# Kernel optimization log

Measured on AMD Instinct MI355X. Metric: run time of the kernel, lower is better.

## Reference

```python
import jax, jax.numpy as jnp
import numpy as np
from jax.scipy.special import ndtri
from jax.scipy.stats import norm

B, C, S = 8192, 1024, 16  # batch, num_classes, sample_size


def setup_inputs() -> dict:
    key = jax.random.key(0)
    k1, k2 = jax.random.split(key)
    logits = jax.random.normal(k1, (B, C), dtype=jnp.float32)
    labels = jax.random.randint(k2, (B,), 0, C, dtype=jnp.int32)
    temperature = jnp.ones((1,), dtype=jnp.float32)
    return {"logits": logits, "labels": labels, "temperature": temperature}


def _exact_loss(logits, labels, temperature, sample_size=S):
    # Global batch-norm of logits (torch .std() is unbiased -> ddof=1).
    logits = (logits - logits.mean()) / jnp.std(logits, ddof=1)
    num_classes = logits.shape[-1]
    # logits_deltas: target logit minus every logit, target column excluded via mask.
    tgt = jnp.take_along_axis(logits, labels[:, None], axis=-1)  # (B, 1)
    delta = (tgt - logits) / temperature[0]                      # (B, C)
    alt_mask = 1.0 - jax.nn.one_hot(labels, num_classes, dtype=logits.dtype)  # 0 at target
    # PositiveNormalProb: P(delta_j + eps_y - eps_j > 0 for all j != y),
    # eps iid N(0,1). Conditioning on eps_y = t gives independent events:
    #   prob = E_{t~N(0,1)}[ prod_j Phi(delta_j + t) ]
    # integrated with sample_size midpoint quantile nodes t_k = Phi^{-1}((k+0.5)/S).
    grid = (jnp.arange(sample_size, dtype=logits.dtype) + 0.5) / sample_size
    t = ndtri(grid)                                              # (S,)
    logcdf = norm.logcdf(delta[:, None, :] + t[None, :, None])   # (B, S, C)
    logp = jnp.sum(logcdf * alt_mask[:, None, :], axis=-1)       # (B, S)
    probs = jnp.mean(jnp.exp(logp), axis=-1)                     # (B,)
    # reduction = 'mean': expected error rate
    return 1.0 - probs.mean()


def reference(logits, labels, temperature):
    return _exact_loss(logits, labels, temperature)
```

## Files before the change

### kernel.cpp

```cpp
#include <hip/hip_runtime.h>
#include <math.h>

#define NB 8192
#define NC 1024
#define NS 16

#define NT   2464
#define NTR  2461
#define C0   48
#define BMAXF 1984.0f
#define UBIAS 978.5f

constexpr int OFFK[16] = {0, 69, 109, 139, 164, 187, 208, 228,
                          248, 268, 289, 312, 337, 367, 407, 476};

#define PSUM  16
#define PSQ   1040
#define RCNT  2064
#define RLIST 3088
#define PART  11280
#define TAB   11408
#define NBLK_MAIN 128

__global__ __launch_bounds__(256) void k_pre(const float* __restrict__ logits,
                                             const int* __restrict__ labels,
                                             float* __restrict__ ws) {
    const int bid = blockIdx.x;
    if (bid >= 1024) {
        int i = (bid - 1024) * 256 + threadIdx.x;
        if (i < NT) {
            int ii = i < NTR ? i : (NTR - 1);
            double x = -9.5 + (double)ii * (1.0 / 128.0);
            ws[TAB + i] = (float)log(0.5 * erfc(-x * 0.70710678118654752440));
        }
        return;
    }
    const int w = threadIdx.x >> 6, l = threadIdx.x & 63;
    const float4* lf4 = (const float4*)logits;
    __shared__ int flags[8];
    __shared__ float bs[4], bss[4];
    float s = 0.0f, ss = 0.0f;
    for (int rr = 0; rr < 2; ++rr) {
        const int row = bid * 8 + w * 2 + rr;
        const float tgt = logits[row * NC + labels[row]];
        int cnt = 0;
        #pragma unroll
        for (int i = 0; i < 4; ++i) {
            float4 v = lf4[row * (NC / 4) + l + 64 * i];
            s  += v.x + v.y + v.z + v.w;
            ss += v.x * v.x + v.y * v.y + v.z * v.z + v.w * v.w;
            cnt += (v.x >= tgt) + (v.y >= tgt) + (v.z >= tgt) + (v.w >= tgt);
        }
        #pragma unroll
        for (int m = 32; m; m >>= 1) cnt += __shfl_xor(cnt, m, 64);
        if (l == 0) flags[w * 2 + rr] = ((cnt - 1) < C0);
    }
    #pragma unroll
    for (int m = 32; m; m >>= 1) {
        s  += __shfl_xor(s,  m, 64);
        ss += __shfl_xor(ss, m, 64);
    }
    if (l == 0) { bs[w] = s; bss[w] = ss; }
    __syncthreads();
    if (threadIdx.x == 0) {
        ws[PSUM + bid] = bs[0] + bs[1] + bs[2] + bs[3];
        ws[PSQ + bid]  = bss[0] + bss[1] + bss[2] + bss[3];
        int* wsi = (int*)ws;
        int n = 0;
        #pragma unroll
        for (int i = 0; i < 8; ++i)
            if (flags[i]) wsi[RLIST + bid * 8 + (n++)] = bid * 8 + i;
        wsi[RCNT + bid] = n;
    }
}

__global__ __launch_bounds__(256) void k_main(const float* __restrict__ logits,
                                              const int* __restrict__ labels,
                                              const float* __restrict__ temp,
                                              float* __restrict__ ws) {
    const int bid = blockIdx.x, tid = threadIdx.x;
    const int* wsi = (const int*)ws;
    const int w = tid >> 6, l = tid & 63;

    __shared__ float lt[NT];
    __shared__ int   P[1024];
    __shared__ int   wtot[4];
    __shared__ float rs[4], rss[4];
    __shared__ float shInv;
    __shared__ float wprob[4];

    float4* lt4 = (float4*)lt;
    const float4* gt4 = (const float4*)(ws + TAB);
    for (int i = tid; i < NT / 4; i += 256) lt4[i] = gt4[i];

    int c4[4];
    const int b4 = tid * 4;
    #pragma unroll
    for (int j = 0; j < 4; ++j) c4[j] = wsi[RCNT + b4 + j];
    int s4 = c4[0] + c4[1] + c4[2] + c4[3];
    int v = s4;
    #pragma unroll
    for (int off = 1; off < 64; off <<= 1) {
        int u = __shfl_up(v, off, 64);
        if (l >= off) v += u;
    }
    if (l == 63) wtot[w] = v;

    float s  = ws[PSUM + tid] + ws[PSUM + 256 + tid] + ws[PSUM + 512 + tid] + ws[PSUM + 768 + tid];
    float ss = ws[PSQ + tid]  + ws[PSQ + 256 + tid]  + ws[PSQ + 512 + tid]  + ws[PSQ + 768 + tid];
    #pragma unroll
    for (int m = 32; m; m >>= 1) {
        s  += __shfl_xor(s,  m, 64);
        ss += __shfl_xor(ss, m, 64);
    }
    if (l == 0) { rs[w] = s; rss[w] = ss; }
    __syncthreads();

    int wbase = 0;
    #pragma unroll
    for (int ww = 0; ww < 4; ++ww) if (ww < w) wbase += wtot[ww];
    int ex = wbase + v - s4;
    P[b4 + 0] = ex;
    P[b4 + 1] = ex + c4[0];
    P[b4 + 2] = ex + c4[0] + c4[1];
    P[b4 + 3] = ex + c4[0] + c4[1] + c4[2];
    const int Ntot = wtot[0] + wtot[1] + wtot[2] + wtot[3];

    if (tid == 0) {
        float S1 = rs[0] + rs[1] + rs[2] + rs[3];
        float S2 = rss[0] + rss[1] + rss[2] + rss[3];
        const float N = (float)NB * (float)NC;
        float var = (S2 - S1 * S1 / N) / (N - 1.0f);
        shInv = 128.0f / (sqrtf(var) * temp[0]);
    }
    __syncthreads();
    const float s128 = shInv;

    const float4* lf4 = (const float4*)logits;
    float waveProb = 0.0f;
    const int gwave = bid * 4 + w;

    for (int i = gwave; i < Ntot; i += NBLK_MAIN * 4) {
        int lo = 0, hi = 1023;
        while (lo < hi) {
            int mid = (lo + hi + 1) >> 1;
            if (P[mid] <= i) lo = mid; else hi = mid - 1;
        }
        const int row = wsi[RLIST + lo * 8 + (i - P[lo])];

        const float tgt = logits[row * NC + labels[row]];
        const float A = fmaf(tgt, s128, UBIAS);
        float a[16];
        #pragma unroll
        for (int k = 0; k < 16; ++k) a[k] = 0.0f;
        #pragma unroll
        for (int ii = 0; ii < 4; ++ii) {
            float4 vv4 = lf4[row * (NC / 4) + l + 64 * ii];
            float vv[4] = {vv4.x, vv4.y, vv4.z, vv4.w};
            #pragma unroll
            for (int j = 0; j < 4; ++j) {
                float u = fmaf(vv[j], -s128, A);
                u = fminf(fmaxf(u, 0.0f), BMAXF);
                int bi = (int)u;
                #pragma unroll
                for (int k = 0; k < 16; ++k) a[k] += lt[bi + OFFK[k]];
            }
        }
        #pragma unroll
        for (int k = 0; k < 16; ++k) {
            #pragma unroll
            for (int m = 32; m; m >>= 1) a[k] += __shfl_xor(a[k], m, 64);
        }
        float uy = fmaf(tgt, -s128, A);
        uy = fminf(fmaxf(uy, 0.0f), BMAXF);
        int by = (int)uy;
        float prob = 0.0f;
        #pragma unroll
        for (int k = 0; k < 16; ++k) prob += __expf(a[k] - lt[by + OFFK[k]]);
        waveProb += prob * (1.0f / 16.0f);
    }

    if (l == 0) wprob[w] = waveProb;
    __syncthreads();
    if (tid == 0) ws[PART + bid] = wprob[0] + wprob[1] + wprob[2] + wprob[3];
}

__global__ __launch_bounds__(128) void k_final(const float* __restrict__ ws,
                                               float* __restrict__ out) {
    const int tid = threadIdx.x;
    float p = ws[PART + tid];
    #pragma unroll
    for (int m = 32; m; m >>= 1) p += __shfl_xor(p, m, 64);
    __shared__ float t[2];
    if ((tid & 63) == 0) t[tid >> 6] = p;
    __syncthreads();
    if (tid == 0) out[0] = 1.0f - (t[0] + t[1]) * (1.0f / (float)NB);
}

extern "C" void kernel_launch(void* const* d_in, const int* in_sizes, int n_in,
                              void* d_out, int out_size, void* d_ws, size_t ws_size,
                              hipStream_t stream) {
    const float* logits = (const float*)d_in[0];
    const int*   labels = (const int*)d_in[1];
    const float* temp   = (const float*)d_in[2];
    float* ws  = (float*)d_ws;
    float* out = (float*)d_out;

    hipLaunchKernelGGL(k_pre,   dim3(1024 + (NT + 255) / 256), dim3(256), 0, stream,
                       logits, labels, ws);
    hipLaunchKernelGGL(k_main,  dim3(NBLK_MAIN), dim3(256), 0, stream,
                       logits, labels, temp, ws);
    hipLaunchKernelGGL(k_final, dim3(1), dim3(128), 0, stream, ws, out);
}
```

Measured before the change: 21.09 us.

## Fuse final reduction into main kernel via atomic ticket and use float table

```diff
diff --git a/kernel.cpp b/kernel.cpp
--- a/kernel.cpp
+++ b/kernel.cpp
@@ -14,6 +14,7 @@
 constexpr int OFFK[16] = {0, 69, 109, 139, 164, 187, 208, 228,
                           248, 268, 289, 312, 337, 367, 407, 476};
 
+#define TICKET 2
 #define PSUM  16
 #define PSQ   1040
 #define RCNT  2064
@@ -22,16 +23,23 @@
 #define TAB   11408
 #define NBLK_MAIN 128
 
+__device__ __forceinline__ float log_ndtr_f(float x) {
+    float e = erfcf(-x * 0.70710678118654752f);
+    if (e > 1e-37f) return __logf(0.5f * e);
+    return -0.5f * x * x - 0.91893853320467274f - __logf(-x);
+}
+
 __global__ __launch_bounds__(256) void k_pre(const float* __restrict__ logits,
                                              const int* __restrict__ labels,
                                              float* __restrict__ ws) {
     const int bid = blockIdx.x;
     if (bid >= 1024) {
+        if (bid == 1024 && threadIdx.x == 0) ((int*)ws)[TICKET] = 0;
         int i = (bid - 1024) * 256 + threadIdx.x;
         if (i < NT) {
             int ii = i < NTR ? i : (NTR - 1);
-            double x = -9.5 + (double)ii * (1.0 / 128.0);
-            ws[TAB + i] = (float)log(0.5 * erfc(-x * 0.70710678118654752440));
+            float x = -9.5f + (float)ii * (1.0f / 128.0f);
+            ws[TAB + i] = log_ndtr_f(x);
         }
         return;
     }
@@ -77,7 +85,8 @@
 __global__ __launch_bounds__(256) void k_main(const float* __restrict__ logits,
                                               const int* __restrict__ labels,
                                               const float* __restrict__ temp,
-                                              float* __restrict__ ws) {
+                                              float* __restrict__ ws,
+                                              float* __restrict__ out) {
     const int bid = blockIdx.x, tid = threadIdx.x;
     const int* wsi = (const int*)ws;
     const int w = tid >> 6, l = tid & 63;
@@ -88,6 +97,7 @@
     __shared__ float rs[4], rss[4];
     __shared__ float shInv;
     __shared__ float wprob[4];
+    __shared__ int   shLast;
 
     float4* lt4 = (float4*)lt;
     const float4* gt4 = (const float4*)(ws + TAB);
@@ -182,19 +192,28 @@
 
     if (l == 0) wprob[w] = waveProb;
     __syncthreads();
-    if (tid == 0) ws[PART + bid] = wprob[0] + wprob[1] + wprob[2] + wprob[3];
-}
-
-__global__ __launch_bounds__(128) void k_final(const float* __restrict__ ws,
-                                               float* __restrict__ out) {
-    const int tid = threadIdx.x;
-    float p = ws[PART + tid];
-    #pragma unroll
-    for (int m = 32; m; m >>= 1) p += __shfl_xor(p, m, 64);
-    __shared__ float t[2];
-    if ((tid & 63) == 0) t[tid >> 6] = p;
-    __syncthreads();
-    if (tid == 0) out[0] = 1.0f - (t[0] + t[1]) * (1.0f / (float)NB);
+
+    if (tid == 0) {
+        float part = wprob[0] + wprob[1] + wprob[2] + wprob[3];
+        __hip_atomic_store(&ws[PART + bid], part, __ATOMIC_RELAXED,
+                           __HIP_MEMORY_SCOPE_AGENT);
+        int t = __hip_atomic_fetch_add((int*)ws + TICKET, 1, __ATOMIC_ACQ_REL,
+                                       __HIP_MEMORY_SCOPE_AGENT);
+        shLast = (t == NBLK_MAIN - 1);
+    }
+    __syncthreads();
+    if (shLast) {
+        float p = 0.0f;
+        if (tid < NBLK_MAIN)
+            p = __hip_atomic_load(&ws[PART + tid], __ATOMIC_RELAXED,
+                                  __HIP_MEMORY_SCOPE_AGENT);
+        #pragma unroll
+        for (int m = 32; m; m >>= 1) p += __shfl_xor(p, m, 64);
+        if (l == 0) wprob[w] = p;
+        __syncthreads();
+        if (tid == 0)
+            out[0] = 1.0f - (wprob[0] + wprob[1]) * (1.0f / (float)NB);
+    }
 }
 
 extern "C" void kernel_launch(void* const* d_in, const int* in_sizes, int n_in,
@@ -206,9 +225,8 @@
     float* ws  = (float*)d_ws;
     float* out = (float*)d_out;
 
-    hipLaunchKernelGGL(k_pre,   dim3(1024 + (NT + 255) / 256), dim3(256), 0, stream,
+    hipLaunchKernelGGL(k_pre,  dim3(1024 + (NT + 255) / 256), dim3(256), 0, stream,
                        logits, labels, ws);
-    hipLaunchKernelGGL(k_main,  dim3(NBLK_MAIN), dim3(256), 0, stream,
-                       logits, labels, temp, ws);
-    hipLaunchKernelGGL(k_final, dim3(1), dim3(128), 0, stream, ws, out);
-}
+    hipLaunchKernelGGL(k_main, dim3(NBLK_MAIN), dim3(256), 0, stream,
+                       logits, labels, temp, ws, out);
+}
```

Result: no change. 21.49 us (+1.9%).

## Flatten selected row list in a scan kernel and run one-wave main blocks

Applied to the files above, without the earlier changes.

```diff
diff --git a/kernel.cpp b/kernel.cpp
--- a/kernel.cpp
+++ b/kernel.cpp
@@ -3,7 +3,6 @@
 
 #define NB 8192
 #define NC 1024
-#define NS 16
 
 #define NT   2464
 #define NTR  2461
@@ -14,13 +13,22 @@
 constexpr int OFFK[16] = {0, 69, 109, 139, 164, 187, 208, 228,
                           248, 268, 289, 312, 337, 367, 407, 476};
 
-#define PSUM  16
-#define PSQ   1040
-#define RCNT  2064
-#define RLIST 3088
-#define PART  11280
-#define TAB   11408
-#define NBLK_MAIN 128
+#define NTOT_I 4
+#define INVS_F 5
+#define PSUM   16
+#define PSQ    1040
+#define RCNT   2064
+#define RLIST  3088
+#define FLAT   11280
+#define PART   19472
+#define TAB    19984
+#define NBLK_MAIN 512
+
+__device__ __forceinline__ float log_ndtr_f(float x) {
+    float e = erfcf(-x * 0.70710678118654752f);
+    if (e > 1e-37f) return __logf(0.5f * e);
+    return -0.5f * x * x - 0.91893853320467274f - __logf(-x);
+}
 
 __global__ __launch_bounds__(256) void k_pre(const float* __restrict__ logits,
                                              const int* __restrict__ labels,
@@ -30,8 +38,8 @@
         int i = (bid - 1024) * 256 + threadIdx.x;
         if (i < NT) {
             int ii = i < NTR ? i : (NTR - 1);
-            double x = -9.5 + (double)ii * (1.0 / 128.0);
-            ws[TAB + i] = (float)log(0.5 * erfc(-x * 0.70710678118654752440));
+            float x = -9.5f + (float)ii * (1.0f / 128.0f);
+            ws[TAB + i] = log_ndtr_f(x);
         }
         return;
     }
@@ -74,24 +82,13 @@
     }
 }
 
-__global__ __launch_bounds__(256) void k_main(const float* __restrict__ logits,
-                                              const int* __restrict__ labels,
-                                              const float* __restrict__ temp,
+__global__ __launch_bounds__(256) void k_scan(const float* __restrict__ temp,
                                               float* __restrict__ ws) {
-    const int bid = blockIdx.x, tid = threadIdx.x;
-    const int* wsi = (const int*)ws;
+    const int tid = threadIdx.x;
     const int w = tid >> 6, l = tid & 63;
-
-    __shared__ float lt[NT];
-    __shared__ int   P[1024];
-    __shared__ int   wtot[4];
+    int* wsi = (int*)ws;
+    __shared__ int wtot[4];
     __shared__ float rs[4], rss[4];
-    __shared__ float shInv;
-    __shared__ float wprob[4];
-
-    float4* lt4 = (float4*)lt;
-    const float4* gt4 = (const float4*)(ws + TAB);
-    for (int i = tid; i < NT / 4; i += 256) lt4[i] = gt4[i];
 
     int c4[4];
     const int b4 = tid * 4;
@@ -119,35 +116,45 @@
     int wbase = 0;
     #pragma unroll
     for (int ww = 0; ww < 4; ++ww) if (ww < w) wbase += wtot[ww];
-    int ex = wbase + v - s4;
-    P[b4 + 0] = ex;
-    P[b4 + 1] = ex + c4[0];
-    P[b4 + 2] = ex + c4[0] + c4[1];
-    P[b4 + 3] = ex + c4[0] + c4[1] + c4[2];
-    const int Ntot = wtot[0] + wtot[1] + wtot[2] + wtot[3];
+    int base = wbase + v - s4;
+    #pragma unroll
+    for (int j = 0; j < 4; ++j) {
+        for (int i = 0; i < c4[j]; ++i)
+            wsi[FLAT + base + i] = wsi[RLIST + (b4 + j) * 8 + i];
+        base += c4[j];
+    }
 
     if (tid == 0) {
+        wsi[NTOT_I] = wtot[0] + wtot[1] + wtot[2] + wtot[3];
         float S1 = rs[0] + rs[1] + rs[2] + rs[3];
         float S2 = rss[0] + rss[1] + rss[2] + rss[3];
         const float N = (float)NB * (float)NC;
         float var = (S2 - S1 * S1 / N) / (N - 1.0f);
-        shInv = 128.0f / (sqrtf(var) * temp[0]);
-    }
-    __syncthreads();
-    const float s128 = shInv;
-
+        ws[INVS_F] = 128.0f / (sqrtf(var) * temp[0]);
+    }
+}
+
+__global__ __launch_bounds__(64) void k_main(const float* __restrict__ logits,
+                                             const int* __restrict__ labels,
+                                             float* __restrict__ ws) {
+    const int bid = blockIdx.x, lane = threadIdx.x;
+    const int* wsi = (const int*)ws;
+    const int Ntot = wsi[NTOT_I];
+    if (bid >= Ntot) {
+        if (lane == 0) ws[PART + bid] = 0.0f;
+        return;
+    }
+    __shared__ float lt[NT];
+    float4* lt4 = (float4*)lt;
+    const float4* gt4 = (const float4*)(ws + TAB);
+    for (int i = lane; i < NT / 4; i += 64) lt4[i] = gt4[i];
+    const float s128 = ws[INVS_F];
     const float4* lf4 = (const float4*)logits;
-    float waveProb = 0.0f;
-    const int gwave = bid * 4 + w;
-
-    for (int i = gwave; i < Ntot; i += NBLK_MAIN * 4) {
-        int lo = 0, hi = 1023;
-        while (lo < hi) {
-            int mid = (lo + hi + 1) >> 1;
-            if (P[mid] <= i) lo = mid; else hi = mid - 1;
-        }
-        const int row = wsi[RLIST + lo * 8 + (i - P[lo])];
-
+    float acc = 0.0f;
+    __syncthreads();
+
+    for (int i = bid; i < Ntot; i += NBLK_MAIN) {
+        const int row = wsi[FLAT + i];
         const float tgt = logits[row * NC + labels[row]];
         const float A = fmaf(tgt, s128, UBIAS);
         float a[16];
@@ -155,8 +162,8 @@
         for (int k = 0; k < 16; ++k) a[k] = 0.0f;
         #pragma unroll
         for (int ii = 0; ii < 4; ++ii) {
-            float4 vv4 = lf4[row * (NC / 4) + l + 64 * ii];
-            float vv[4] = {vv4.x, vv4.y, vv4.z, vv4.w};
+            float4 v = lf4[row * (NC / 4) + lane + 64 * ii];
+            float vv[4] = {v.x, v.y, v.z, v.w};
             #pragma unroll
             for (int j = 0; j < 4; ++j) {
                 float u = fmaf(vv[j], -s128, A);
@@ -171,30 +178,30 @@
             #pragma unroll
             for (int m = 32; m; m >>= 1) a[k] += __shfl_xor(a[k], m, 64);
         }
-        float uy = fmaf(tgt, -s128, A);
-        uy = fminf(fmaxf(uy, 0.0f), BMAXF);
-        int by = (int)uy;
-        float prob = 0.0f;
-        #pragma unroll
-        for (int k = 0; k < 16; ++k) prob += __expf(a[k] - lt[by + OFFK[k]]);
-        waveProb += prob * (1.0f / 16.0f);
-    }
-
-    if (l == 0) wprob[w] = waveProb;
-    __syncthreads();
-    if (tid == 0) ws[PART + bid] = wprob[0] + wprob[1] + wprob[2] + wprob[3];
-}
-
-__global__ __launch_bounds__(128) void k_final(const float* __restrict__ ws,
+        if (lane == 0) {
+            float uy = fmaf(tgt, -s128, A);
+            uy = fminf(fmaxf(uy, 0.0f), BMAXF);
+            int by = (int)uy;
+            float prob = 0.0f;
+            #pragma unroll
+            for (int k = 0; k < 16; ++k) prob += __expf(a[k] - lt[by + OFFK[k]]);
+            acc += prob * (1.0f / 16.0f);
+        }
+    }
+    if (lane == 0) ws[PART + bid] = acc;
+}
+
+__global__ __launch_bounds__(256) void k_final(const float* __restrict__ ws,
                                                float* __restrict__ out) {
     const int tid = threadIdx.x;
-    float p = ws[PART + tid];
+    float p = ws[PART + tid] + ws[PART + 256 + tid];
     #pragma unroll
     for (int m = 32; m; m >>= 1) p += __shfl_xor(p, m, 64);
-    __shared__ float t[2];
+    __shared__ float t[4];
     if ((tid & 63) == 0) t[tid >> 6] = p;
     __syncthreads();
-    if (tid == 0) out[0] = 1.0f - (t[0] + t[1]) * (1.0f / (float)NB);
+    if (tid == 0)
+        out[0] = 1.0f - (t[0] + t[1] + t[2] + t[3]) * (1.0f / (float)NB);
 }
 
 extern "C" void kernel_launch(void* const* d_in, const int* in_sizes, int n_in,
@@ -208,7 +215,8 @@
 
     hipLaunchKernelGGL(k_pre,   dim3(1024 + (NT + 255) / 256), dim3(256), 0, stream,
                        logits, labels, ws);
-    hipLaunchKernelGGL(k_main,  dim3(NBLK_MAIN), dim3(256), 0, stream,
-                       logits, labels, temp, ws);
-    hipLaunchKernelGGL(k_final, dim3(1), dim3(128), 0, stream, ws, out);
-}
+    hipLaunchKernelGGL(k_scan,  dim3(1),         dim3(256), 0, stream, temp, ws);
+    hipLaunchKernelGGL(k_main,  dim3(NBLK_MAIN), dim3(64),  0, stream,
+                       logits, labels, ws);
+    hipLaunchKernelGGL(k_final, dim3(1),         dim3(256), 0, stream, ws, out);
+}
```

New measurement: 24.96 us. 18.4% more time.
